# Kernel tuning notes

Hardware: AMD Instinct MI355X
Metric: run time of the kernel (lower is better)

Reference implementation:

```python
import jax, jax.numpy as jnp
import numpy as np
from jax import lax

GAMMA = 0.99
LAM = 0.95
CLIP_PARAM = 0.2
VALUE_LOSS_COEF = 0.5
ENTROPY_COEF = 0.01
EPS = 1e-09

B, T = 4096, 2048


def setup_inputs() -> dict:
    key = jax.random.key(0)
    ks = jax.random.split(key, 6)
    rewards = jax.random.normal(ks[0], (B, T), dtype=jnp.float32)
    values = jax.random.normal(ks[1], (B, T + 1), dtype=jnp.float32)
    ref_probs = jax.random.uniform(ks[2], (B, T), dtype=jnp.float32)
    old_probs = jax.random.uniform(ks[3], (B, T), dtype=jnp.float32)
    curr_probs = jax.random.uniform(ks[4], (B, T), dtype=jnp.float32)
    # episode-continuation masks: mostly 1, occasional 0 (episode boundary)
    masks = (jax.random.uniform(ks[5], (B, T)) > 0.02).astype(jnp.float32)
    return {"rewards": rewards, "values": values, "ref_probs": ref_probs,
            "old_probs": old_probs, "curr_probs": curr_probs, "masks": masks}


def compute_gae(rewards, values, masks, gamma, lam):
    # single fused reverse scan over time; per-step state is (B,)
    def step(carry, xs):
        r, v, v_next, m = xs
        delta = r + gamma * v_next * m - v
        adv = delta + gamma * lam * m * carry
        return adv, adv

    xs = (rewards.T, values[:, :-1].T, values[:, 1:].T, masks.T)  # each (T, B)
    _, advs = lax.scan(step, jnp.zeros(rewards.shape[0], rewards.dtype), xs, reverse=True)
    advantages = advs.T  # (B, T)
    returns = advantages + values[:, :-1]
    return advantages, returns


def reference(rewards, values, ref_probs, old_probs, curr_probs, masks):
    advantages, returns = compute_gae(rewards, values, masks, GAMMA, LAM)
    # torch .std() is unbiased (ddof=1)
    advantages = (advantages - advantages.mean()) / (advantages.std(ddof=1) + EPS)
    ratios = curr_probs / (old_probs + EPS)
    surr1 = ratios * advantages
    surr2 = jnp.clip(ratios, 1.0 - CLIP_PARAM, 1.0 + CLIP_PARAM) * advantages
    ppo_loss = -jnp.minimum(surr1, surr2).mean()
    value_loss = jnp.mean((returns - values[:, :-1]) ** 2)
    entropy_loss = -jnp.mean(curr_probs * jnp.log(curr_probs + EPS))
    total_loss = ppo_loss + VALUE_LOSS_COEF * value_loss + ENTROPY_COEF * entropy_loss
    return (total_loss, ppo_loss, VALUE_LOSS_COEF * value_loss, ENTROPY_COEF * entropy_loss)
```

## Files before the change

kernel.cpp:

```cpp
#include <hip/hip_runtime.h>
#include <math.h>


#define GAMMA     0.99f
#define LAM       0.95f
#define CLIP_LO   0.8f
#define CLIP_HI   1.2f
#define EPSF      1e-9f

constexpr int BB = 4096;
constexpr int TT = 2048;
constexpr long long NN = (long long)BB * TT;
constexpr int GAE_BLOCKS = BB / 2;
constexpr int PPO_BLOCKS = 2048;

struct Stats { float mean; float inv; double sum2; };
static constexpr size_t GAE_PART_OFF = 64;
static constexpr size_t PPO_PART_OFF = GAE_PART_OFF + GAE_BLOCKS * sizeof(float2);
static constexpr size_t ADV_OFF      = PPO_PART_OFF + PPO_BLOCKS * sizeof(float2);

__device__ __forceinline__ unsigned bf16_rne(float x) {
    unsigned u = __float_as_uint(x);
    u += 0x7FFFu + ((u >> 16) & 1u);
    return u >> 16;
}

__global__ __launch_bounds__(256, 4) void gae_kernel(
    const float* __restrict__ rewards,
    const float* __restrict__ values,
    const float* __restrict__ masks,
    uint4* __restrict__ advb,
    float2* __restrict__ partials)
{
    const int tid  = threadIdx.x;
    const int lane = tid & 63;
    const int wave = tid >> 6;
    const int t0   = tid * 8;
    const int row0 = blockIdx.x * 2;
    const int row1 = row0 + 1;

    __shared__ float2 wTa[4], wTb[4];
    __shared__ float  wr1[4], wr2[4];

    const float* ra = rewards + (size_t)row0 * TT;
    const float* ma = masks   + (size_t)row0 * TT;
    const float* va_ = values + (size_t)row0 * (TT + 1);
    const float* rb = rewards + (size_t)row1 * TT;
    const float* mb = masks   + (size_t)row1 * TT;
    const float* vb_ = values + (size_t)row1 * (TT + 1);

    float4 ra0 = *(const float4*)(ra + t0);
    float4 ra1 = *(const float4*)(ra + t0 + 4);
    float4 ma0 = *(const float4*)(ma + t0);
    float4 ma1 = *(const float4*)(ma + t0 + 4);
    float4 rb0 = *(const float4*)(rb + t0);
    float4 rb1 = *(const float4*)(rb + t0 + 4);
    float4 mb0 = *(const float4*)(mb + t0);
    float4 mb1 = *(const float4*)(mb + t0 + 4);
    float va[9], vb[9];
#pragma unroll
    for (int j = 0; j < 9; ++j) va[j] = va_[t0 + j];
#pragma unroll
    for (int j = 0; j < 9; ++j) vb[j] = vb_[t0 + j];

    float rA[8] = {ra0.x, ra0.y, ra0.z, ra0.w, ra1.x, ra1.y, ra1.z, ra1.w};
    float mA[8] = {ma0.x, ma0.y, ma0.z, ma0.w, ma1.x, ma1.y, ma1.z, ma1.w};
    float rB[8] = {rb0.x, rb0.y, rb0.z, rb0.w, rb1.x, rb1.y, rb1.z, rb1.w};
    float mB[8] = {mb0.x, mb0.y, mb0.z, mb0.w, mb1.x, mb1.y, mb1.z, mb1.w};

    float laA[8], SA[8], laB[8], SB[8];
    {
        float d[8], c[8];
#pragma unroll
        for (int j = 0; j < 8; ++j) {
            d[j] = rA[j] + GAMMA * va[j + 1] * mA[j] - va[j];
            c[j] = (GAMMA * LAM) * mA[j];
        }
        laA[7] = d[7]; SA[7] = c[7];
#pragma unroll
        for (int j = 6; j >= 0; --j) { laA[j] = d[j] + c[j] * laA[j + 1]; SA[j] = c[j] * SA[j + 1]; }
    }
    {
        float d[8], c[8];
#pragma unroll
        for (int j = 0; j < 8; ++j) {
            d[j] = rB[j] + GAMMA * vb[j + 1] * mB[j] - vb[j];
            c[j] = (GAMMA * LAM) * mB[j];
        }
        laB[7] = d[7]; SB[7] = c[7];
#pragma unroll
        for (int j = 6; j >= 0; --j) { laB[j] = d[j] + c[j] * laB[j + 1]; SB[j] = c[j] * SB[j + 1]; }
    }

    float Aa = SA[0], Ba = laA[0];
    float Ab = SB[0], Bb = laB[0];
#pragma unroll
    for (int d = 1; d < 64; d <<= 1) {
        float A2a = __shfl_down(Aa, d, 64), B2a = __shfl_down(Ba, d, 64);
        float A2b = __shfl_down(Ab, d, 64), B2b = __shfl_down(Bb, d, 64);
        if (lane + d < 64) {
            Ba = Ba + Aa * B2a;  Aa = Aa * A2a;
            Bb = Bb + Ab * B2b;  Ab = Ab * A2b;
        }
    }
    if (lane == 0) { wTa[wave] = make_float2(Aa, Ba); wTb[wave] = make_float2(Ab, Bb); }
    __syncthreads();
    float Ca = 0.0f, Cb = 0.0f;
    for (int ww = 3; ww > wave; --ww) {
        Ca = wTa[ww].y + wTa[ww].x * Ca;
        Cb = wTb[ww].y + wTb[ww].x * Cb;
    }
    float A1a = __shfl_down(Aa, 1, 64), B1a = __shfl_down(Ba, 1, 64);
    float A1b = __shfl_down(Ab, 1, 64), B1b = __shfl_down(Bb, 1, 64);
    float carA = (lane < 63) ? (B1a + A1a * Ca) : Ca;
    float carB = (lane < 63) ? (B1b + A1b * Cb) : Cb;

    float s1 = 0.f, s2 = 0.f;
    unsigned ha[8], hb[8];
#pragma unroll
    for (int j = 0; j < 8; ++j) {
        float a = laA[j] + SA[j] * carA;
        s1 += a; s2 += a * a;
        ha[j] = bf16_rne(a);
        float b = laB[j] + SB[j] * carB;
        s1 += b; s2 += b * b;
        hb[j] = bf16_rne(b);
    }
    uint4 pa = {ha[0] | (ha[1] << 16), ha[2] | (ha[3] << 16),
                ha[4] | (ha[5] << 16), ha[6] | (ha[7] << 16)};
    uint4 pb = {hb[0] | (hb[1] << 16), hb[2] | (hb[3] << 16),
                hb[4] | (hb[5] << 16), hb[6] | (hb[7] << 16)};
    advb[row0 * 256 + tid] = pa;
    advb[row1 * 256 + tid] = pb;

#pragma unroll
    for (int off = 32; off > 0; off >>= 1) {
        s1 += __shfl_down(s1, off, 64);
        s2 += __shfl_down(s2, off, 64);
    }
    if (lane == 0) { wr1[wave] = s1; wr2[wave] = s2; }
    __syncthreads();
    if (tid == 0) {
        float2 p = {wr1[0] + wr1[1] + wr1[2] + wr1[3],
                    wr2[0] + wr2[1] + wr2[2] + wr2[3]};
        partials[blockIdx.x] = p;
    }
}

__global__ __launch_bounds__(256) void finalize_stats(
    const float2* __restrict__ gp, Stats* __restrict__ stats)
{
    const int tid = threadIdx.x;
    __shared__ double l1[256], l2[256];
    double s1 = 0.0, s2 = 0.0;
    for (int i = tid; i < GAE_BLOCKS; i += 256) {
        float2 p = gp[i];
        s1 += (double)p.x;
        s2 += (double)p.y;
    }
    l1[tid] = s1; l2[tid] = s2;
    __syncthreads();
    for (int st = 128; st > 0; st >>= 1) {
        if (tid < st) { l1[tid] += l1[tid + st]; l2[tid] += l2[tid + st]; }
        __syncthreads();
    }
    if (tid == 0) {
        double S1 = l1[0], S2 = l2[0];
        double mean = S1 / (double)NN;
        double var  = (S2 - S1 * S1 / (double)NN) / (double)(NN - 1);
        stats->mean = (float)mean;
        stats->inv  = (float)(1.0 / (sqrt(var) + 1e-9));
        stats->sum2 = S2;
    }
}

__global__ __launch_bounds__(256, 8) void ppo_kernel(
    const float* __restrict__ adv_bf16,
    const float* __restrict__ oldp,
    const float* __restrict__ currp,
    const Stats* __restrict__ stats,
    float2* __restrict__ partials)
{
    const float mean = stats->mean;
    const float inv  = stats->inv;
    const int tid = threadIdx.x;
    const int b   = blockIdx.x;

    const uint2*  a2 = (const uint2*)adv_bf16;
    const float4* o4 = (const float4*)oldp;
    const float4* c4 = (const float4*)currp;

    uint2  Aq[4]; float4 Of[4], Cf[4];
#pragma unroll
    for (int k = 0; k < 4; ++k) {
        int i = b * 1024 + k * 256 + tid;
        Aq[k] = a2[i]; Of[k] = o4[i]; Cf[k] = c4[i];
    }

    float sm = 0.f, se = 0.f;
#pragma unroll
    for (int k = 0; k < 4; ++k) {
        float av[4] = {__uint_as_float(Aq[k].x << 16),
                       __uint_as_float(Aq[k].x & 0xFFFF0000u),
                       __uint_as_float(Aq[k].y << 16),
                       __uint_as_float(Aq[k].y & 0xFFFF0000u)};
        float ov[4] = {Of[k].x, Of[k].y, Of[k].z, Of[k].w};
        float cv[4] = {Cf[k].x, Cf[k].y, Cf[k].z, Cf[k].w};
#pragma unroll
        for (int j = 0; j < 4; ++j) {
            float an    = (av[j] - mean) * inv;
            float ratio = cv[j] * __builtin_amdgcn_rcpf(ov[j] + EPSF);
            float rc    = fminf(fmaxf(ratio, CLIP_LO), CLIP_HI);
            sm += fminf(ratio * an, rc * an);
            se += cv[j] * __logf(cv[j] + EPSF);
        }
    }

#pragma unroll
    for (int off = 32; off > 0; off >>= 1) {
        sm += __shfl_down(sm, off, 64);
        se += __shfl_down(se, off, 64);
    }
    __shared__ float w1[4], w2[4];
    const int wave = tid >> 6, lane = tid & 63;
    if (lane == 0) { w1[wave] = sm; w2[wave] = se; }
    __syncthreads();
    if (tid == 0) {
        float2 p = {w1[0] + w1[1] + w1[2] + w1[3],
                    w2[0] + w2[1] + w2[2] + w2[3]};
        partials[b] = p;
    }
}

__global__ __launch_bounds__(256) void finalize_out(
    const float2* __restrict__ pp,
    const Stats* __restrict__ stats,
    float* __restrict__ out)
{
    const int tid = threadIdx.x;
    __shared__ double l1[256], l2[256];
    double s1 = 0.0, s2 = 0.0;
    for (int i = tid; i < PPO_BLOCKS; i += 256) {
        float2 p = pp[i];
        s1 += (double)p.x;
        s2 += (double)p.y;
    }
    l1[tid] = s1; l2[tid] = s2;
    __syncthreads();
    for (int st = 128; st > 0; st >>= 1) {
        if (tid < st) { l1[tid] += l1[tid + st]; l2[tid] += l2[tid + st]; }
        __syncthreads();
    }
    if (tid == 0) {
        double invN = 1.0 / (double)NN;
        double vl   = 0.5  * (stats->sum2 * invN);
        double ppo  = -(l1[0] * invN);
        double ent  = -0.01 * (l2[0] * invN);
        out[0] = (float)(ppo + vl + ent);
        out[1] = (float)ppo;
        out[2] = (float)vl;
        out[3] = (float)ent;
    }
}

extern "C" void kernel_launch(void* const* d_in, const int* in_sizes, int n_in,
                              void* d_out, int out_size, void* d_ws, size_t ws_size,
                              hipStream_t stream) {
    const float* rewards = (const float*)d_in[0];
    const float* values  = (const float*)d_in[1];
    const float* oldp    = (const float*)d_in[3];
    const float* currp   = (const float*)d_in[4];
    const float* masks   = (const float*)d_in[5];

    Stats*  stats = (Stats*)d_ws;
    float2* gaep  = (float2*)((char*)d_ws + GAE_PART_OFF);
    float2* ppop  = (float2*)((char*)d_ws + PPO_PART_OFF);
    uint4*  advb  = (uint4*)((char*)d_ws + ADV_OFF);
    float*  out   = (float*)d_out;

    gae_kernel<<<GAE_BLOCKS, 256, 0, stream>>>(rewards, values, masks, advb, gaep);
    finalize_stats<<<1, 256, 0, stream>>>(gaep, stats);
    ppo_kernel<<<PPO_BLOCKS, 256, 0, stream>>>((const float*)advb, oldp, currp, stats, ppop);
    finalize_out<<<1, 256, 0, stream>>>(ppop, stats, out);
}
```

Measured before the change: 203.5 us.

## Process one row per GAE block, split into two half-row scan segments

```diff
diff --git a/kernel.cpp b/kernel.cpp
--- a/kernel.cpp
+++ b/kernel.cpp
@@ -11,7 +11,7 @@
 constexpr int BB = 4096;
 constexpr int TT = 2048;
 constexpr long long NN = (long long)BB * TT;
-constexpr int GAE_BLOCKS = BB / 2;
+constexpr int GAE_BLOCKS = BB;
 constexpr int PPO_BLOCKS = 2048;
 
 struct Stats { float mean; float inv; double sum2; };
@@ -29,67 +29,67 @@
     const float* __restrict__ rewards,
     const float* __restrict__ values,
     const float* __restrict__ masks,
-    uint4* __restrict__ advb,
+    uint2* __restrict__ advb,
     float2* __restrict__ partials)
 {
+    const int row  = blockIdx.x;
     const int tid  = threadIdx.x;
     const int lane = tid & 63;
     const int wave = tid >> 6;
-    const int t0   = tid * 8;
-    const int row0 = blockIdx.x * 2;
-    const int row1 = row0 + 1;
-
+
+    __shared__ float  lvx[513];
     __shared__ float2 wTa[4], wTb[4];
     __shared__ float  wr1[4], wr2[4];
 
-    const float* ra = rewards + (size_t)row0 * TT;
-    const float* ma = masks   + (size_t)row0 * TT;
-    const float* va_ = values + (size_t)row0 * (TT + 1);
-    const float* rb = rewards + (size_t)row1 * TT;
-    const float* mb = masks   + (size_t)row1 * TT;
-    const float* vb_ = values + (size_t)row1 * (TT + 1);
-
-    float4 ra0 = *(const float4*)(ra + t0);
-    float4 ra1 = *(const float4*)(ra + t0 + 4);
-    float4 ma0 = *(const float4*)(ma + t0);
-    float4 ma1 = *(const float4*)(ma + t0 + 4);
-    float4 rb0 = *(const float4*)(rb + t0);
-    float4 rb1 = *(const float4*)(rb + t0 + 4);
-    float4 mb0 = *(const float4*)(mb + t0);
-    float4 mb1 = *(const float4*)(mb + t0 + 4);
-    float va[9], vb[9];
-#pragma unroll
-    for (int j = 0; j < 9; ++j) va[j] = va_[t0 + j];
-#pragma unroll
-    for (int j = 0; j < 9; ++j) vb[j] = vb_[t0 + j];
-
-    float rA[8] = {ra0.x, ra0.y, ra0.z, ra0.w, ra1.x, ra1.y, ra1.z, ra1.w};
-    float mA[8] = {ma0.x, ma0.y, ma0.z, ma0.w, ma1.x, ma1.y, ma1.z, ma1.w};
-    float rB[8] = {rb0.x, rb0.y, rb0.z, rb0.w, rb1.x, rb1.y, rb1.z, rb1.w};
-    float mB[8] = {mb0.x, mb0.y, mb0.z, mb0.w, mb1.x, mb1.y, mb1.z, mb1.w};
-
-    float laA[8], SA[8], laB[8], SB[8];
+    const float* rrow = rewards + (size_t)row * TT;
+    const float* mrow = masks   + (size_t)row * TT;
+    const float* vrow = values  + (size_t)row * (TT + 1);
+
+    float4 rA = *(const float4*)(rrow + 4 * tid);
+    float4 mA = *(const float4*)(mrow + 4 * tid);
+    float4 rB = *(const float4*)(rrow + 1024 + 4 * tid);
+    float4 mB = *(const float4*)(mrow + 1024 + 4 * tid);
+    float vA[4], vB[4];
+#pragma unroll
+    for (int j = 0; j < 4; ++j) vA[j] = vrow[4 * tid + j];
+#pragma unroll
+    for (int j = 0; j < 4; ++j) vB[j] = vrow[1024 + 4 * tid + j];
+
+    lvx[tid]       = vA[0];
+    lvx[256 + tid] = vB[0];
+    if (tid == 255) lvx[512] = vrow[2048];
+    __syncthreads();
+    const float vA4 = lvx[tid + 1];
+    const float vB4 = lvx[257 + tid];
+
+    float laA[4], SA[4], laB[4], SB[4];
     {
-        float d[8], c[8];
-#pragma unroll
-        for (int j = 0; j < 8; ++j) {
-            d[j] = rA[j] + GAMMA * va[j + 1] * mA[j] - va[j];
-            c[j] = (GAMMA * LAM) * mA[j];
-        }
-        laA[7] = d[7]; SA[7] = c[7];
-#pragma unroll
-        for (int j = 6; j >= 0; --j) { laA[j] = d[j] + c[j] * laA[j + 1]; SA[j] = c[j] * SA[j + 1]; }
+        float rr[4] = {rA.x, rA.y, rA.z, rA.w};
+        float mm[4] = {mA.x, mA.y, mA.z, mA.w};
+        float vn[4] = {vA[1], vA[2], vA[3], vA4};
+        float d[4], c[4];
+#pragma unroll
+        for (int j = 0; j < 4; ++j) {
+            d[j] = rr[j] + GAMMA * vn[j] * mm[j] - vA[j];
+            c[j] = (GAMMA * LAM) * mm[j];
+        }
+        laA[3] = d[3]; SA[3] = c[3];
+#pragma unroll
+        for (int j = 2; j >= 0; --j) { laA[j] = d[j] + c[j] * laA[j + 1]; SA[j] = c[j] * SA[j + 1]; }
     }
     {
-        float d[8], c[8];
-#pragma unroll
-        for (int j = 0; j < 8; ++j) {
-            d[j] = rB[j] + GAMMA * vb[j + 1] * mB[j] - vb[j];
-            c[j] = (GAMMA * LAM) * mB[j];
-        }
-        laB[7] = d[7]; SB[7] = c[7];
-#pragma unroll
-        for (int j = 6; j >= 0; --j) { laB[j] = d[j] + c[j] * laB[j + 1]; SB[j] = c[j] * SB[j + 1]; }
+        float rr[4] = {rB.x, rB.y, rB.z, rB.w};
+        float mm[4] = {mB.x, mB.y, mB.z, mB.w};
+        float vn[4] = {vB[1], vB[2], vB[3], vB4};
+        float d[4], c[4];
+#pragma unroll
+        for (int j = 0; j < 4; ++j) {
+            d[j] = rr[j] + GAMMA * vn[j] * mm[j] - vB[j];
+            c[j] = (GAMMA * LAM) * mm[j];
+        }
+        laB[3] = d[3]; SB[3] = c[3];
+#pragma unroll
+        for (int j = 2; j >= 0; --j) { laB[j] = d[j] + c[j] * laB[j + 1]; SB[j] = c[j] * SB[j + 1]; }
     }
 
     float Aa = SA[0], Ba = laA[0];
@@ -105,20 +105,25 @@
     }
     if (lane == 0) { wTa[wave] = make_float2(Aa, Ba); wTb[wave] = make_float2(Ab, Bb); }
     __syncthreads();
-    float Ca = 0.0f, Cb = 0.0f;
-    for (int ww = 3; ww > wave; --ww) {
-        Ca = wTa[ww].y + wTa[ww].x * Ca;
-        Cb = wTb[ww].y + wTb[ww].x * Cb;
-    }
+
+    float V = 0.0f, Cb = 0.0f;
+#pragma unroll
+    for (int ww = 3; ww >= 0; --ww) {
+        if (ww == wave) Cb = V;
+        V = wTb[ww].y + wTb[ww].x * V;
+    }
+    float Ca = V;
+    for (int ww = 3; ww > wave; --ww) Ca = wTa[ww].y + wTa[ww].x * Ca;
+
     float A1a = __shfl_down(Aa, 1, 64), B1a = __shfl_down(Ba, 1, 64);
     float A1b = __shfl_down(Ab, 1, 64), B1b = __shfl_down(Bb, 1, 64);
     float carA = (lane < 63) ? (B1a + A1a * Ca) : Ca;
     float carB = (lane < 63) ? (B1b + A1b * Cb) : Cb;
 
     float s1 = 0.f, s2 = 0.f;
-    unsigned ha[8], hb[8];
-#pragma unroll
-    for (int j = 0; j < 8; ++j) {
+    unsigned ha[4], hb[4];
+#pragma unroll
+    for (int j = 0; j < 4; ++j) {
         float a = laA[j] + SA[j] * carA;
         s1 += a; s2 += a * a;
         ha[j] = bf16_rne(a);
@@ -126,12 +131,10 @@
         s1 += b; s2 += b * b;
         hb[j] = bf16_rne(b);
     }
-    uint4 pa = {ha[0] | (ha[1] << 16), ha[2] | (ha[3] << 16),
-                ha[4] | (ha[5] << 16), ha[6] | (ha[7] << 16)};
-    uint4 pb = {hb[0] | (hb[1] << 16), hb[2] | (hb[3] << 16),
-                hb[4] | (hb[5] << 16), hb[6] | (hb[7] << 16)};
-    advb[row0 * 256 + tid] = pa;
-    advb[row1 * 256 + tid] = pb;
+    uint2 pa = {ha[0] | (ha[1] << 16), ha[2] | (ha[3] << 16)};
+    uint2 pb = {hb[0] | (hb[1] << 16), hb[2] | (hb[3] << 16)};
+    advb[row * 512 + tid]       = pa;
+    advb[row * 512 + 256 + tid] = pb;
 
 #pragma unroll
     for (int off = 32; off > 0; off >>= 1) {
@@ -143,7 +146,7 @@
     if (tid == 0) {
         float2 p = {wr1[0] + wr1[1] + wr1[2] + wr1[3],
                     wr2[0] + wr2[1] + wr2[2] + wr2[3]};
-        partials[blockIdx.x] = p;
+        partials[row] = p;
     }
 }
 
@@ -275,7 +278,7 @@
     Stats*  stats = (Stats*)d_ws;
     float2* gaep  = (float2*)((char*)d_ws + GAE_PART_OFF);
     float2* ppop  = (float2*)((char*)d_ws + PPO_PART_OFF);
-    uint4*  advb  = (uint4*)((char*)d_ws + ADV_OFF);
+    uint2*  advb  = (uint2*)((char*)d_ws + ADV_OFF);
     float*  out   = (float*)d_out;
 
     gae_kernel<<<GAE_BLOCKS, 256, 0, stream>>>(rewards, values, masks, advb, gaep);
```

Result: no change. 205.9 us (+1.2%).
